# Kernel tuning notes

Measured on AMD Instinct MI355X. Metric: run time of the kernel, lower is better.

Reference implementation:

```python
import jax, jax.numpy as jnp
import numpy as np

H = 16
D_MODEL = 1024
D_K = D_MODEL // H


def setup_inputs() -> dict:
    key = jax.random.key(0)
    ks = jax.random.split(key, 10)
    B, S = 2, 2048
    q = jax.random.normal(ks[0], (B, S, D_MODEL), dtype=jnp.float32)
    k = jax.random.normal(ks[1], (B, S, D_MODEL), dtype=jnp.float32)
    v = jax.random.normal(ks[2], (B, S, D_MODEL), dtype=jnp.float32)
    mask = jax.random.randint(ks[3], (B, 1, S), 0, 2, dtype=jnp.int32)
    s = 1.0 / np.sqrt(D_MODEL)
    w_q = jax.random.normal(ks[4], (D_MODEL, D_MODEL), dtype=jnp.float32) * s
    b_q = jnp.zeros((D_MODEL,), dtype=jnp.float32)
    w_v = jax.random.normal(ks[5], (D_MODEL, D_MODEL), dtype=jnp.float32) * s
    b_v = jnp.zeros((D_MODEL,), dtype=jnp.float32)
    w_o = jax.random.normal(ks[6], (D_MODEL, D_MODEL), dtype=jnp.float32) * s
    b_o = jnp.zeros((D_MODEL,), dtype=jnp.float32)
    return {"q": q, "k": k, "v": v, "mask": mask,
            "w_q": w_q, "b_q": b_q, "w_v": w_v, "b_v": b_v,
            "w_o": w_o, "b_o": b_o}


def _split_heads(x, B):
    # [B, S, D] -> [B, H, S, d_k]
    return x.reshape(B, -1, H, D_K).transpose(0, 2, 1, 3)


def reference(q, k, v, mask, w_q, b_q, w_v, b_v, w_o, b_o):
    B = q.shape[0]
    # NOTE: source uses w_q for BOTH q and k (w_k is dead code) — reproduced faithfully.
    qh = _split_heads(q @ w_q.T + b_q, B)
    kh = _split_heads(k @ w_q.T + b_q, B)
    vh = _split_heads(v @ w_v.T + b_v, B)
    scores = jnp.einsum('bhqd,bhkd->bhqk', qh, kh) * (1.0 / np.sqrt(D_K))
    # mask [B,1,S] -> unsqueeze(1) -> [B,1,1,S], broadcast over heads and query dim
    m = mask[:, None, :, :]
    scores = jnp.where(m == 0, -jnp.inf, scores)
    attn = jax.nn.softmax(scores, axis=-1)  # dropout is identity (eval / p=0)
    out = jnp.einsum('bhqk,bhkd->bhqd', attn, vh)
    out = out.transpose(0, 2, 1, 3).reshape(B, -1, D_MODEL)
    out = out @ w_o.T + b_o
    return out, attn
```

## Files before the change

### kernel.cpp

```cpp
#include <hip/hip_runtime.h>

#define S_LEN 2048
#define DMODEL 1024
#define NH 16
#define DK 64
#define BATCH 2
#define BS (BATCH * S_LEN)

typedef _Float16 f16;
typedef _Float16 f16x8 __attribute__((ext_vector_type(8)));
typedef _Float16 f16x4 __attribute__((ext_vector_type(4)));
typedef float f32x4 __attribute__((ext_vector_type(4)));

__device__ __forceinline__ f32x4 mfma16(f16x8 a, f16x8 b, f32x4 c) {
  return __builtin_amdgcn_mfma_f32_16x16x32_f16(a, b, c, 0, 0, 0);
}

__global__ __launch_bounds__(256) void cvt6(
    const float* __restrict__ a0, const float* __restrict__ a1,
    const float* __restrict__ a2, const float* __restrict__ a3,
    const float* __restrict__ a4, const float* __restrict__ a5,
    f16* __restrict__ d0, f16* __restrict__ d1, f16* __restrict__ d2,
    f16* __restrict__ d3, f16* __restrict__ d4, f16* __restrict__ d5) {
  const int y = blockIdx.y;
  const float* s;
  f16* d;
  switch (y) {
    case 0: s = a0; d = d0; break;
    case 1: s = a1; d = d1; break;
    case 2: s = a2; d = d2; break;
    case 3: s = a3; d = d3; break;
    case 4: s = a4; d = d4; break;
    default: s = a5; d = d5; break;
  }
  const int n = (y < 3) ? BS * DMODEL : DMODEL * DMODEL;
  const int idx = (blockIdx.x * 256 + threadIdx.x) * 4;
  if (idx >= n) return;
  const float4 v = *reinterpret_cast<const float4*>(&s[idx]);
  f16x4 h = {(f16)v.x, (f16)v.y, (f16)v.z, (f16)v.w};
  *reinterpret_cast<f16x4*>(&d[idx]) = h;
}

template <int MODE>
__device__ __forceinline__ void gemm_body16(const f16* __restrict__ A,
                                            const f16* __restrict__ W,
                                            const float* __restrict__ bias,
                                            void* __restrict__ outp, float scale,
                                            f16 (*As)[72], f16 (*Ws)[72]) {
  const int t = threadIdx.x;
  const int m0 = blockIdx.y * 128;
  const int n0 = blockIdx.x * 128;
  const int wave = t >> 6, lane = t & 63;
  const int wr = wave >> 1, wc = wave & 1;
  const int lcol = lane & 15, kq = lane >> 4;

  f32x4 acc[4][4];
  const f32x4 zero = {0.f, 0.f, 0.f, 0.f};
#pragma unroll
  for (int i = 0; i < 4; ++i)
#pragma unroll
    for (int j = 0; j < 4; ++j) acc[i][j] = zero;

  for (int k0 = 0; k0 < DMODEL; k0 += 64) {
#pragma unroll
    for (int i = 0; i < 4; ++i) {
      const int f = t + i * 256;
      const int r = f >> 3, c = (f & 7) << 3;
      *reinterpret_cast<f16x8*>(&As[r][c]) =
          *reinterpret_cast<const f16x8*>(&A[(size_t)(m0 + r) * DMODEL + k0 + c]);
      *reinterpret_cast<f16x8*>(&Ws[r][c]) =
          *reinterpret_cast<const f16x8*>(&W[(size_t)(n0 + r) * DMODEL + k0 + c]);
    }
    __syncthreads();
#pragma unroll
    for (int ks = 0; ks < 2; ++ks) {
      f16x8 af[4], bf[4];
#pragma unroll
      for (int fr = 0; fr < 4; ++fr)
        af[fr] = *reinterpret_cast<const f16x8*>(
            &As[wr * 64 + fr * 16 + lcol][ks * 32 + kq * 8]);
#pragma unroll
      for (int fc = 0; fc < 4; ++fc)
        bf[fc] = *reinterpret_cast<const f16x8*>(
            &Ws[wc * 64 + fc * 16 + lcol][ks * 32 + kq * 8]);
#pragma unroll
      for (int fr = 0; fr < 4; ++fr)
#pragma unroll
        for (int fc = 0; fc < 4; ++fc)
          acc[fr][fc] = mfma16(af[fr], bf[fc], acc[fr][fc]);
    }
    __syncthreads();
  }

#pragma unroll
  for (int fc = 0; fc < 4; ++fc) {
    const int gj = n0 + wc * 64 + fc * 16 + lcol;
    const float bv = bias[gj];
#pragma unroll
    for (int fr = 0; fr < 4; ++fr) {
#pragma unroll
      for (int r = 0; r < 4; ++r) {
        const int gi = m0 + wr * 64 + fr * 16 + kq * 4 + r;
        const float val = (acc[fr][fc][r] + bv) * scale;
        if constexpr (MODE == 0) {
          const int b = gi >> 11, s = gi & 2047, h = gj >> 6, dk = gj & 63;
          ((f16*)outp)[(((size_t)(b * NH + h) * S_LEN) + s) * DK + dk] = (f16)val;
        } else if constexpr (MODE == 1) {
          const int b = gi >> 11, s = gi & 2047, h = gj >> 6, dk = gj & 63;
          ((f16*)outp)[(((size_t)(b * NH + h) * DK) + dk) * S_LEN + s] = (f16)val;
        } else {
          ((float*)outp)[(size_t)gi * DMODEL + gj] = val;
        }
      }
    }
  }
}

__global__ __launch_bounds__(256, 2) void qkv_gemm(
    const f16* __restrict__ qf, const f16* __restrict__ kf,
    const f16* __restrict__ vf, const f16* __restrict__ wq,
    const float* __restrict__ b_q, const f16* __restrict__ wv,
    const float* __restrict__ b_v, f16* __restrict__ qh, f16* __restrict__ kh,
    f16* __restrict__ vhT) {
  __shared__ f16 As[128][72];
  __shared__ f16 Ws[128][72];
  if (blockIdx.z == 0)
    gemm_body16<0>(qf, wq, b_q, qh, 0.125f, As, Ws);
  else if (blockIdx.z == 1)
    gemm_body16<0>(kf, wq, b_q, kh, 1.0f, As, Ws);
  else
    gemm_body16<1>(vf, wv, b_v, vhT, 1.0f, As, Ws);
}

__global__ __launch_bounds__(256, 2) void gemm_out(const f16* __restrict__ A,
                                                   const f16* __restrict__ W,
                                                   const float* __restrict__ bias,
                                                   float* __restrict__ outp) {
  __shared__ f16 As[128][72];
  __shared__ f16 Ws[128][72];
  gemm_body16<2>(A, W, bias, outp, 1.0f, As, Ws);
}

__global__ __launch_bounds__(256, 4) void attn_fused(
    const f16* __restrict__ qh, const f16* __restrict__ kh,
    const f16* __restrict__ vhT, const int* __restrict__ mask,
    float* __restrict__ attn, f16* __restrict__ ctx) {
  __shared__ f16 Ps[4][16][72];
  __shared__ int msk[S_LEN];
  const int t = threadIdx.x;
  const int bh = blockIdx.y, b = bh >> 4, h = bh & 15;
  const int i0 = blockIdx.x * 64;
  const int wave = t >> 6, lane = t & 63;
  const int lcol = lane & 15, kq = lane >> 4;
  const int rbase = i0 + wave * 16;
  const f16* Q = qh + (size_t)bh * S_LEN * DK;
  const f16* K = kh + (size_t)bh * S_LEN * DK;
  const f16* V = vhT + (size_t)bh * DK * S_LEN;
  float* Sc = attn + (size_t)bh * S_LEN * S_LEN;

  for (int i = t; i < S_LEN; i += 256) msk[i] = mask[b * S_LEN + i];

  f16x8 aq[2];
#pragma unroll
  for (int ks = 0; ks < 2; ++ks)
    aq[ks] = *reinterpret_cast<const f16x8*>(
        &Q[(size_t)(rbase + lcol) * DK + ks * 32 + kq * 8]);

  float l_acc[4] = {0.f, 0.f, 0.f, 0.f};
  f32x4 o[4];
  const f32x4 zero = {0.f, 0.f, 0.f, 0.f};
#pragma unroll
  for (int d = 0; d < 4; ++d) o[d] = zero;

  __syncthreads();

  for (int j0 = 0; j0 < S_LEN; j0 += 64) {
#pragma unroll
    for (int jt = 0; jt < 4; ++jt) {
      const f16* Krow = &K[(size_t)(j0 + jt * 16 + lcol) * DK + kq * 8];
      const f16x8 bk0 = *reinterpret_cast<const f16x8*>(Krow);
      const f16x8 bk1 = *reinterpret_cast<const f16x8*>(Krow + 32);
      const int mv = msk[j0 + jt * 16 + lcol];
      f32x4 c = zero;
      c = mfma16(aq[0], bk0, c);
      c = mfma16(aq[1], bk1, c);
#pragma unroll
      for (int r = 0; r < 4; ++r) {
        const float pun = mv ? __expf(c[r]) : 0.f;
        l_acc[r] += pun;
        Ps[wave][kq * 4 + r][jt * 16 + lcol] = (f16)pun;
      }
    }
#pragma unroll
    for (int ks = 0; ks < 2; ++ks) {
      const f16x8 ap =
          *reinterpret_cast<const f16x8*>(&Ps[wave][lcol][ks * 32 + kq * 8]);
      f16x8 bv[4];
#pragma unroll
      for (int d = 0; d < 4; ++d)
        bv[d] = *reinterpret_cast<const f16x8*>(
            &V[(size_t)(d * 16 + lcol) * S_LEN + j0 + ks * 32 + kq * 8]);
#pragma unroll
      for (int d = 0; d < 4; ++d) o[d] = mfma16(ap, bv[d], o[d]);
    }
  }

  float il[4];
#pragma unroll
  for (int r = 0; r < 4; ++r) {
    float es = l_acc[r];
#pragma unroll
    for (int off = 1; off < 16; off <<= 1) es += __shfl_xor(es, off);
    il[r] = 1.0f / es;
  }

  for (int j0 = 0; j0 < S_LEN; j0 += 64) {
#pragma unroll
    for (int jt = 0; jt < 4; ++jt) {
      const f16* Krow = &K[(size_t)(j0 + jt * 16 + lcol) * DK + kq * 8];
      const f16x8 bk0 = *reinterpret_cast<const f16x8*>(Krow);
      const f16x8 bk1 = *reinterpret_cast<const f16x8*>(Krow + 32);
      const int mv = msk[j0 + jt * 16 + lcol];
      f32x4 c = zero;
      c = mfma16(aq[0], bk0, c);
      c = mfma16(aq[1], bk1, c);
#pragma unroll
      for (int r = 0; r < 4; ++r) {
        const float p = mv ? __expf(c[r]) * il[r] : 0.f;
        Sc[((size_t)(rbase + kq * 4 + r) << 11) + j0 + jt * 16 + lcol] = p;
      }
    }
  }

#pragma unroll
  for (int d = 0; d < 4; ++d) {
    const int dk = d * 16 + lcol;
#pragma unroll
    for (int r = 0; r < 4; ++r) {
      const int s = rbase + kq * 4 + r;
      ctx[(size_t)(b * S_LEN + s) * DMODEL + h * DK + dk] = (f16)(o[d][r] * il[r]);
    }
  }
}

extern "C" void kernel_launch(void* const* d_in, const int* in_sizes, int n_in,
                              void* d_out, int out_size, void* d_ws, size_t ws_size,
                              hipStream_t stream) {
  const float* q = (const float*)d_in[0];
  const float* k = (const float*)d_in[1];
  const float* v = (const float*)d_in[2];
  const int* mask = (const int*)d_in[3];
  const float* w_q = (const float*)d_in[4];
  const float* b_q = (const float*)d_in[5];
  const float* w_v = (const float*)d_in[6];
  const float* b_v = (const float*)d_in[7];
  const float* w_o = (const float*)d_in[8];
  const float* b_o = (const float*)d_in[9];

  float* out = (float*)d_out;
  float* attn = out + (size_t)BS * DMODEL;

  f16* qf = (f16*)d_ws;
  f16* kf = qf + (size_t)BS * DMODEL;
  f16* vf = kf + (size_t)BS * DMODEL;
  f16* wqf = vf + (size_t)BS * DMODEL;
  f16* wvf = wqf + (size_t)DMODEL * DMODEL;
  f16* wof = wvf + (size_t)DMODEL * DMODEL;
  f16* qh = wof + (size_t)DMODEL * DMODEL;
  f16* kh = qh + (size_t)BS * DMODEL;
  f16* vhT = kh + (size_t)BS * DMODEL;
  f16* ctx = vhT + (size_t)BS * DMODEL;

  cvt6<<<dim3(4096, 6), 256, 0, stream>>>(q, k, v, w_q, w_v, w_o, qf, kf, vf,
                                          wqf, wvf, wof);
  qkv_gemm<<<dim3(8, 32, 3), 256, 0, stream>>>(qf, kf, vf, wqf, b_q, wvf, b_v,
                                               qh, kh, vhT);
  attn_fused<<<dim3(32, 32), 256, 0, stream>>>(qh, kh, vhT, mask, attn, ctx);
  gemm_out<<<dim3(8, 32), 256, 0, stream>>>(ctx, wof, b_o, out);
}
```

Measured before the change: 995.4 us.

## Split attention key range across wave pairs with 32-row tiles and LDS reduction

```diff
diff --git a/kernel.cpp b/kernel.cpp
--- a/kernel.cpp
+++ b/kernel.cpp
@@ -6,6 +6,7 @@
 #define DK 64
 #define BATCH 2
 #define BS (BATCH * S_LEN)
+#define KHALF 1024
 
 typedef _Float16 f16;
 typedef _Float16 f16x8 __attribute__((ext_vector_type(8)));
@@ -116,7 +117,7 @@
   }
 }
 
-__global__ __launch_bounds__(256, 2) void qkv_gemm(
+__global__ __launch_bounds__(256, 3) void qkv_gemm(
     const f16* __restrict__ qf, const f16* __restrict__ kf,
     const f16* __restrict__ vf, const f16* __restrict__ wq,
     const float* __restrict__ b_q, const f16* __restrict__ wv,
@@ -145,101 +146,158 @@
     const f16* __restrict__ qh, const f16* __restrict__ kh,
     const f16* __restrict__ vhT, const int* __restrict__ mask,
     float* __restrict__ attn, f16* __restrict__ ctx) {
-  __shared__ f16 Ps[4][16][72];
-  __shared__ int msk[S_LEN];
+  __shared__ __align__(16) unsigned char smem[18432];
   const int t = threadIdx.x;
   const int bh = blockIdx.y, b = bh >> 4, h = bh & 15;
   const int i0 = blockIdx.x * 64;
   const int wave = t >> 6, lane = t & 63;
+  const int rh = wave & 1, khf = wave >> 1;
   const int lcol = lane & 15, kq = lane >> 4;
-  const int rbase = i0 + wave * 16;
+  const int rbase = i0 + rh * 32;
+  const int jbase = khf * KHALF;
+  f16 (*Ps)[72] = reinterpret_cast<f16(*)[72]>(smem + wave * 4608);
+  float (*Ost)[68] = reinterpret_cast<float(*)[68]>(smem);
+  float* lred = reinterpret_cast<float*>(smem + 17408);
+
   const f16* Q = qh + (size_t)bh * S_LEN * DK;
   const f16* K = kh + (size_t)bh * S_LEN * DK;
   const f16* V = vhT + (size_t)bh * DK * S_LEN;
+  const int* msk = mask + b * S_LEN;
   float* Sc = attn + (size_t)bh * S_LEN * S_LEN;
 
-  for (int i = t; i < S_LEN; i += 256) msk[i] = mask[b * S_LEN + i];
-
-  f16x8 aq[2];
-#pragma unroll
-  for (int ks = 0; ks < 2; ++ks)
-    aq[ks] = *reinterpret_cast<const f16x8*>(
-        &Q[(size_t)(rbase + lcol) * DK + ks * 32 + kq * 8]);
-
-  float l_acc[4] = {0.f, 0.f, 0.f, 0.f};
-  f32x4 o[4];
+  f16x8 aq[2][2];
+#pragma unroll
+  for (int rt = 0; rt < 2; ++rt)
+#pragma unroll
+    for (int ks = 0; ks < 2; ++ks)
+      aq[rt][ks] = *reinterpret_cast<const f16x8*>(
+          &Q[(size_t)(rbase + rt * 16 + lcol) * DK + ks * 32 + kq * 8]);
+
+  float l_acc[2][4];
+  f32x4 o[2][4];
   const f32x4 zero = {0.f, 0.f, 0.f, 0.f};
 #pragma unroll
-  for (int d = 0; d < 4; ++d) o[d] = zero;
-
-  __syncthreads();
-
-  for (int j0 = 0; j0 < S_LEN; j0 += 64) {
+  for (int rt = 0; rt < 2; ++rt) {
+#pragma unroll
+    for (int r = 0; r < 4; ++r) l_acc[rt][r] = 0.f;
+#pragma unroll
+    for (int d = 0; d < 4; ++d) o[rt][d] = zero;
+  }
+
+  for (int j0 = jbase; j0 < jbase + KHALF; j0 += 64) {
 #pragma unroll
     for (int jt = 0; jt < 4; ++jt) {
       const f16* Krow = &K[(size_t)(j0 + jt * 16 + lcol) * DK + kq * 8];
       const f16x8 bk0 = *reinterpret_cast<const f16x8*>(Krow);
       const f16x8 bk1 = *reinterpret_cast<const f16x8*>(Krow + 32);
       const int mv = msk[j0 + jt * 16 + lcol];
-      f32x4 c = zero;
-      c = mfma16(aq[0], bk0, c);
-      c = mfma16(aq[1], bk1, c);
-#pragma unroll
-      for (int r = 0; r < 4; ++r) {
-        const float pun = mv ? __expf(c[r]) : 0.f;
-        l_acc[r] += pun;
-        Ps[wave][kq * 4 + r][jt * 16 + lcol] = (f16)pun;
+#pragma unroll
+      for (int rt = 0; rt < 2; ++rt) {
+        f32x4 c = zero;
+        c = mfma16(aq[rt][0], bk0, c);
+        c = mfma16(aq[rt][1], bk1, c);
+#pragma unroll
+        for (int r = 0; r < 4; ++r) {
+          const float pun = mv ? __expf(c[r]) : 0.f;
+          l_acc[rt][r] += pun;
+          Ps[rt * 16 + kq * 4 + r][jt * 16 + lcol] = (f16)pun;
+        }
       }
     }
 #pragma unroll
     for (int ks = 0; ks < 2; ++ks) {
-      const f16x8 ap =
-          *reinterpret_cast<const f16x8*>(&Ps[wave][lcol][ks * 32 + kq * 8]);
-      f16x8 bv[4];
+      f16x8 ap[2], bv[4];
+#pragma unroll
+      for (int rt = 0; rt < 2; ++rt)
+        ap[rt] = *reinterpret_cast<const f16x8*>(
+            &Ps[rt * 16 + lcol][ks * 32 + kq * 8]);
 #pragma unroll
       for (int d = 0; d < 4; ++d)
         bv[d] = *reinterpret_cast<const f16x8*>(
             &V[(size_t)(d * 16 + lcol) * S_LEN + j0 + ks * 32 + kq * 8]);
 #pragma unroll
-      for (int d = 0; d < 4; ++d) o[d] = mfma16(ap, bv[d], o[d]);
-    }
-  }
-
-  float il[4];
-#pragma unroll
-  for (int r = 0; r < 4; ++r) {
-    float es = l_acc[r];
-#pragma unroll
-    for (int off = 1; off < 16; off <<= 1) es += __shfl_xor(es, off);
-    il[r] = 1.0f / es;
-  }
-
-  for (int j0 = 0; j0 < S_LEN; j0 += 64) {
+      for (int rt = 0; rt < 2; ++rt)
+#pragma unroll
+        for (int d = 0; d < 4; ++d) o[rt][d] = mfma16(ap[rt], bv[d], o[rt][d]);
+    }
+  }
+
+#pragma unroll
+  for (int rt = 0; rt < 2; ++rt)
+#pragma unroll
+    for (int r = 0; r < 4; ++r) {
+      float es = l_acc[rt][r];
+#pragma unroll
+      for (int off = 1; off < 16; off <<= 1) es += __shfl_xor(es, off);
+      l_acc[rt][r] = es;
+    }
+
+  __syncthreads();
+
+  if (lcol == 0) {
+#pragma unroll
+    for (int rt = 0; rt < 2; ++rt)
+#pragma unroll
+      for (int r = 0; r < 4; ++r)
+        lred[khf * 64 + rh * 32 + rt * 16 + kq * 4 + r] = l_acc[rt][r];
+  }
+  if (khf == 1) {
+#pragma unroll
+    for (int rt = 0; rt < 2; ++rt)
+#pragma unroll
+      for (int d = 0; d < 4; ++d)
+#pragma unroll
+        for (int r = 0; r < 4; ++r)
+          Ost[rh * 32 + rt * 16 + kq * 4 + r][d * 16 + lcol] = o[rt][d][r];
+  }
+  __syncthreads();
+
+  float il[2][4];
+#pragma unroll
+  for (int rt = 0; rt < 2; ++rt)
+#pragma unroll
+    for (int r = 0; r < 4; ++r) {
+      const int rl = rh * 32 + rt * 16 + kq * 4 + r;
+      il[rt][r] = 1.0f / (lred[rl] + lred[64 + rl]);
+    }
+
+  for (int j0 = jbase; j0 < jbase + KHALF; j0 += 64) {
 #pragma unroll
     for (int jt = 0; jt < 4; ++jt) {
       const f16* Krow = &K[(size_t)(j0 + jt * 16 + lcol) * DK + kq * 8];
       const f16x8 bk0 = *reinterpret_cast<const f16x8*>(Krow);
       const f16x8 bk1 = *reinterpret_cast<const f16x8*>(Krow + 32);
       const int mv = msk[j0 + jt * 16 + lcol];
-      f32x4 c = zero;
-      c = mfma16(aq[0], bk0, c);
-      c = mfma16(aq[1], bk1, c);
-#pragma unroll
-      for (int r = 0; r < 4; ++r) {
-        const float p = mv ? __expf(c[r]) * il[r] : 0.f;
-        Sc[((size_t)(rbase + kq * 4 + r) << 11) + j0 + jt * 16 + lcol] = p;
+#pragma unroll
+      for (int rt = 0; rt < 2; ++rt) {
+        f32x4 c = zero;
+        c = mfma16(aq[rt][0], bk0, c);
+        c = mfma16(aq[rt][1], bk1, c);
+#pragma unroll
+        for (int r = 0; r < 4; ++r) {
+          const float p = mv ? __expf(c[r]) * il[rt][r] : 0.f;
+          Sc[((size_t)(rbase + rt * 16 + kq * 4 + r) << 11) + j0 + jt * 16 +
+             lcol] = p;
+        }
       }
     }
   }
 
-#pragma unroll
-  for (int d = 0; d < 4; ++d) {
-    const int dk = d * 16 + lcol;
-#pragma unroll
-    for (int r = 0; r < 4; ++r) {
-      const int s = rbase + kq * 4 + r;
-      ctx[(size_t)(b * S_LEN + s) * DMODEL + h * DK + dk] = (f16)(o[d][r] * il[r]);
-    }
+  if (khf == 0) {
+#pragma unroll
+    for (int rt = 0; rt < 2; ++rt)
+#pragma unroll
+      for (int d = 0; d < 4; ++d) {
+        const int dk = d * 16 + lcol;
+#pragma unroll
+        for (int r = 0; r < 4; ++r) {
+          const int rl = rh * 32 + rt * 16 + kq * 4 + r;
+          const float ov = o[rt][d][r] + Ost[rl][dk];
+          const int s = rbase + rt * 16 + kq * 4 + r;
+          ctx[(size_t)(b * S_LEN + s) * DMODEL + h * DK + dk] =
+              (f16)(ov * il[rt][r]);
+        }
+      }
   }
 }
 
```

New measurement: 932.3 us. 1.07x faster.
